# Optimization experiments

Hardware: AMD Instinct MI355X
Metric: run time of the kernel (lower is better)

The kernel has to match this reference:

```python
import jax, jax.numpy as jnp
import numpy as np

N = 100000   # nodes
E = 600000   # edges
D_IN, D_H, D_OUT = 128, 128, 128


def glorot(key, shape):
    lim = float(np.sqrt(6.0 / (shape[0] + shape[1])))
    return jax.random.uniform(key, shape, jnp.float32, -lim, lim)


def setup_inputs() -> dict:
    key = jax.random.key(0)
    k1, k2, k3, k4 = jax.random.split(key, 4)
    x = jax.random.normal(k1, (N, D_IN), jnp.float32)
    edge_index = jax.random.randint(k2, (2, E), 0, N, jnp.int64)
    W1 = glorot(k3, (D_IN, D_H))
    b1 = jnp.zeros((D_H,), jnp.float32)
    W2 = glorot(k4, (D_H, D_OUT))
    b2 = jnp.zeros((D_OUT,), jnp.float32)
    return {"x": x, "W1": W1, "b1": b1, "W2": W2, "b2": b2, "edge_index": edge_index}


def gcn_conv(x, W, b, src, dst, n):
    # GCNConv: D^{-1/2}(A+I)D^{-1/2} X W + b  (self loops already in src/dst)
    h = x @ W                                   # [N, d_out]
    ones = jnp.ones(src.shape[0], h.dtype)
    deg = jax.ops.segment_sum(ones, dst, num_segments=n)      # in-degree incl self loop
    dinv = jnp.where(deg > 0, jax.lax.rsqrt(deg), 0.0)        # deg^{-1/2}
    norm = dinv[src] * dinv[dst]                              # [E+N]
    msgs = h[src] * norm[:, None]                             # gather + scale
    out = jax.ops.segment_sum(msgs, dst, num_segments=n)      # scatter-add to targets
    return out + b


def reference(x, W1, b1, W2, b2, edge_index):
    loop = jnp.arange(N, dtype=edge_index.dtype)
    src = jnp.concatenate([edge_index[0], loop])
    dst = jnp.concatenate([edge_index[1], loop])
    h = gcn_conv(x, W1, b1, src, dst, N)
    h = jax.nn.relu(h)  # dropout is a no-op in eval mode
    return gcn_conv(h, W2, b2, src, dst, N)
```

## Files before the change

kernel.cpp:

```cpp
#include <hip/hip_runtime.h>

#define NFEAT 128

typedef __attribute__((ext_vector_type(8))) short bf16x8;
typedef __attribute__((ext_vector_type(4))) float f32x4;

__device__ inline ushort f2b(float v) {
  unsigned u = __builtin_bit_cast(unsigned, v);
  unsigned r = (u + 0x7FFFu + ((u >> 16) & 1u)) >> 16;
  return (ushort)r;
}


__global__ __launch_bounds__(256) void k_hist(const int* __restrict__ dst,
                                              int* __restrict__ cnt, int E) {
  int i = blockIdx.x * 256 + threadIdx.x;
  if (i < E) atomicAdd(&cnt[dst[i]], 1);
}

__global__ __launch_bounds__(256) void k_dinv(const int* __restrict__ cnt,
                                              float* __restrict__ dinv, int n) {
  int i = blockIdx.x * 256 + threadIdx.x;
  if (i < n) dinv[i] = rsqrtf((float)(cnt[i] + 1));
}

__global__ __launch_bounds__(256) void k_scan_blocks(const int* __restrict__ cnt,
                                                     int* __restrict__ rowptr,
                                                     int* __restrict__ bsum, int n) {
  __shared__ int s[256];
  int tid = threadIdx.x;
  int idx = blockIdx.x * 1024 + tid * 4;
  int v[4];
  int sum = 0;
#pragma unroll
  for (int j = 0; j < 4; j++) {
    v[j] = (idx + j < n) ? cnt[idx + j] : 0;
    sum += v[j];
  }
  s[tid] = sum;
  __syncthreads();
  for (int off = 1; off < 256; off <<= 1) {
    int t = (tid >= off) ? s[tid - off] : 0;
    __syncthreads();
    s[tid] += t;
    __syncthreads();
  }
  if (tid == 255) bsum[blockIdx.x] = s[255];
  int run = s[tid] - sum;
#pragma unroll
  for (int j = 0; j < 4; j++) {
    if (idx + j < n) rowptr[idx + j] = run;
    run += v[j];
  }
}

__global__ __launch_bounds__(128) void k_scan_sums(int* __restrict__ bsum, int nb) {
  __shared__ int s[128];
  int tid = threadIdx.x;
  int v = (tid < nb) ? bsum[tid] : 0;
  s[tid] = v;
  __syncthreads();
  for (int off = 1; off < 128; off <<= 1) {
    int t = (tid >= off) ? s[tid - off] : 0;
    __syncthreads();
    s[tid] += t;
    __syncthreads();
  }
  if (tid < nb) bsum[tid] = s[tid] - v;
}

__global__ __launch_bounds__(256) void k_scan_add(int* __restrict__ rowptr,
                                                  const int* __restrict__ bsum,
                                                  int n, int e_total) {
  int i = blockIdx.x * 256 + threadIdx.x;
  if (i < n) rowptr[i] += bsum[i >> 10];
  if (i == 0) rowptr[n] = e_total;
}

__global__ __launch_bounds__(256) void k_scatter(const int* __restrict__ src,
                                                 const int* __restrict__ dst,
                                                 const int* __restrict__ rowptr,
                                                 const float* __restrict__ dinv,
                                                 int* __restrict__ cursor,
                                                 int2* __restrict__ csr2, int E) {
  int i = blockIdx.x * 256 + threadIdx.x;
  if (i < E) {
    int d = dst[i];
    int s = src[i];
    int p = atomicAdd(&cursor[d], 1);
    int2 v;
    v.x = s;
    v.y = __float_as_int(dinv[s]);
    csr2[rowptr[d] + p] = v;
  }
}


__global__ __launch_bounds__(256) void k_cast_x(const float* __restrict__ x,
                                                ushort* __restrict__ xb, int total8) {
  int i = blockIdx.x * 256 + threadIdx.x;
  if (i >= total8) return;
  const float4* p = (const float4*)(x + (size_t)i * 8);
  float4 a = p[0], b = p[1];
  uint4 o;
  o.x = f2b(a.x) | ((unsigned)f2b(a.y) << 16);
  o.y = f2b(a.z) | ((unsigned)f2b(a.w) << 16);
  o.z = f2b(b.x) | ((unsigned)f2b(b.y) << 16);
  o.w = f2b(b.z) | ((unsigned)f2b(b.w) << 16);
  *(uint4*)(xb + (size_t)i * 8) = o;
}

__global__ __launch_bounds__(256) void k_cast_wt(const float* __restrict__ W,
                                                 ushort* __restrict__ WT) {
  int idx = blockIdx.x * 256 + threadIdx.x;
  int k = idx >> 7, nn = idx & 127;
  WT[nn * 128 + k] = f2b(W[idx]);
}


__global__ __launch_bounds__(256) void k_gemm_bf16(const ushort* __restrict__ A,
                                                   const ushort* __restrict__ WT,
                                                   ushort* __restrict__ out, int n) {
  __shared__ ushort sW[128][136];
  int tid = threadIdx.x;
  {
    int r = tid >> 1, hh = tid & 1;
    const uint4* srcp = (const uint4*)(WT + r * 128 + hh * 64);
    uint4* dstp = (uint4*)(&sW[r][hh * 64]);
#pragma unroll
    for (int j = 0; j < 8; j++) dstp[j] = srcp[j];
  }
  __syncthreads();

  int wave = tid >> 6;
  int lane = tid & 63;
  int l16 = lane & 15;
  int quad = lane >> 4;
  int rowBase = blockIdx.x * 128 + wave * 32;

  bf16x8 afrag[2][4];
#pragma unroll
  for (int rt = 0; rt < 2; rt++) {
    int row = rowBase + rt * 16 + l16;
    row = min(row, n - 1);
    const ushort* Ap = A + (size_t)row * NFEAT + quad * 8;
#pragma unroll
    for (int ks = 0; ks < 4; ks++) afrag[rt][ks] = *(const bf16x8*)(Ap + ks * 32);
  }

#pragma unroll
  for (int ct = 0; ct < 8; ct++) {
    bf16x8 bfrag[4];
#pragma unroll
    for (int ks = 0; ks < 4; ks++)
      bfrag[ks] = *(const bf16x8*)(&sW[ct * 16 + l16][ks * 32 + quad * 8]);
    f32x4 acc[2] = {{0.f, 0.f, 0.f, 0.f}, {0.f, 0.f, 0.f, 0.f}};
#pragma unroll
    for (int rt = 0; rt < 2; rt++)
#pragma unroll
      for (int ks = 0; ks < 4; ks++)
        acc[rt] = __builtin_amdgcn_mfma_f32_16x16x32_bf16(afrag[rt][ks], bfrag[ks],
                                                          acc[rt], 0, 0, 0);
#pragma unroll
    for (int rt = 0; rt < 2; rt++)
#pragma unroll
      for (int r = 0; r < 4; r++) {
        int row = rowBase + rt * 16 + quad * 4 + r;
        if (row < n) out[(size_t)row * NFEAT + ct * 16 + l16] = f2b(acc[rt][r]);
      }
  }
}


__global__ __launch_bounds__(256) void k_agg_bf16(const ushort* __restrict__ h,
                                                  const float* __restrict__ dinv,
                                                  const int* __restrict__ rowptr,
                                                  const int2* __restrict__ csr2,
                                                  const float* __restrict__ bias,
                                                  ushort* __restrict__ out_bf,
                                                  float* __restrict__ out_f32,
                                                  int n, int relu_bf) {
  int node = blockIdx.x * 8 + (threadIdx.x >> 5);
  if (node >= n) return;
  int lane = threadIdx.x & 31;
  int c = lane * 4;
  float di = dinv[node];

  uint2 hv = *(const uint2*)(h + (size_t)node * NFEAT + c);
  float a0 = di * __uint_as_float(hv.x << 16);
  float a1 = di * __uint_as_float(hv.x & 0xffff0000u);
  float a2 = di * __uint_as_float(hv.y << 16);
  float a3 = di * __uint_as_float(hv.y & 0xffff0000u);

  int e = rowptr[node], end = rowptr[node + 1];
  for (; e + 3 < end; e += 4) {
    int2 p0 = csr2[e], p1 = csr2[e + 1], p2 = csr2[e + 2], p3 = csr2[e + 3];
    uint2 h0 = *(const uint2*)(h + (size_t)p0.x * NFEAT + c);
    uint2 h1 = *(const uint2*)(h + (size_t)p1.x * NFEAT + c);
    uint2 h2 = *(const uint2*)(h + (size_t)p2.x * NFEAT + c);
    uint2 h3 = *(const uint2*)(h + (size_t)p3.x * NFEAT + c);
    float w0 = __int_as_float(p0.y), w1 = __int_as_float(p1.y);
    float w2 = __int_as_float(p2.y), w3 = __int_as_float(p3.y);
    a0 = fmaf(w0, __uint_as_float(h0.x << 16), a0);
    a1 = fmaf(w0, __uint_as_float(h0.x & 0xffff0000u), a1);
    a2 = fmaf(w0, __uint_as_float(h0.y << 16), a2);
    a3 = fmaf(w0, __uint_as_float(h0.y & 0xffff0000u), a3);
    a0 = fmaf(w1, __uint_as_float(h1.x << 16), a0);
    a1 = fmaf(w1, __uint_as_float(h1.x & 0xffff0000u), a1);
    a2 = fmaf(w1, __uint_as_float(h1.y << 16), a2);
    a3 = fmaf(w1, __uint_as_float(h1.y & 0xffff0000u), a3);
    a0 = fmaf(w2, __uint_as_float(h2.x << 16), a0);
    a1 = fmaf(w2, __uint_as_float(h2.x & 0xffff0000u), a1);
    a2 = fmaf(w2, __uint_as_float(h2.y << 16), a2);
    a3 = fmaf(w2, __uint_as_float(h2.y & 0xffff0000u), a3);
    a0 = fmaf(w3, __uint_as_float(h3.x << 16), a0);
    a1 = fmaf(w3, __uint_as_float(h3.x & 0xffff0000u), a1);
    a2 = fmaf(w3, __uint_as_float(h3.y << 16), a2);
    a3 = fmaf(w3, __uint_as_float(h3.y & 0xffff0000u), a3);
  }
  for (; e < end; ++e) {
    int2 p0 = csr2[e];
    uint2 h0 = *(const uint2*)(h + (size_t)p0.x * NFEAT + c);
    float w0 = __int_as_float(p0.y);
    a0 = fmaf(w0, __uint_as_float(h0.x << 16), a0);
    a1 = fmaf(w0, __uint_as_float(h0.x & 0xffff0000u), a1);
    a2 = fmaf(w0, __uint_as_float(h0.y << 16), a2);
    a3 = fmaf(w0, __uint_as_float(h0.y & 0xffff0000u), a3);
  }

  float4 b = *(const float4*)(bias + c);
  float o0 = fmaf(di, a0, b.x);
  float o1 = fmaf(di, a1, b.y);
  float o2 = fmaf(di, a2, b.z);
  float o3 = fmaf(di, a3, b.w);
  if (relu_bf) {
    o0 = fmaxf(o0, 0.f); o1 = fmaxf(o1, 0.f);
    o2 = fmaxf(o2, 0.f); o3 = fmaxf(o3, 0.f);
    uint2 pk;
    pk.x = f2b(o0) | ((unsigned)f2b(o1) << 16);
    pk.y = f2b(o2) | ((unsigned)f2b(o3) << 16);
    *(uint2*)(out_bf + (size_t)node * NFEAT + c) = pk;
  } else {
    float4 o = {o0, o1, o2, o3};
    *(float4*)(out_f32 + (size_t)node * NFEAT + c) = o;
  }
}


extern "C" void kernel_launch(void* const* d_in, const int* in_sizes, int n_in,
                              void* d_out, int out_size, void* d_ws, size_t ws_size,
                              hipStream_t stream) {
  const float* x = (const float*)d_in[0];
  const float* W1 = (const float*)d_in[1];
  const float* b1 = (const float*)d_in[2];
  const float* W2 = (const float*)d_in[3];
  const float* b2 = (const float*)d_in[4];
  const int* ei = (const int*)d_in[5];

  const int N = in_sizes[0] / NFEAT;
  const int E = in_sizes[5] / 2;
  const int* srcIdx = ei;
  const int* dstIdx = ei + E;

  char* p = (char*)d_ws;
  auto alloc = [&](size_t bytes) {
    char* r = p;
    p += (bytes + 255) & ~(size_t)255;
    return r;
  };
  int* cnt = (int*)alloc((size_t)N * 4);
  int* cursor = (int*)alloc((size_t)N * 4);
  float* dinv = (float*)alloc((size_t)N * 4);
  int* rowptr = (int*)alloc((size_t)(N + 1) * 4);
  int* bsum = (int*)alloc(512);
  int2* csr2 = (int2*)alloc((size_t)E * 8);
  ushort* WT1 = (ushort*)alloc(NFEAT * NFEAT * 2);
  ushort* WT2 = (ushort*)alloc(NFEAT * NFEAT * 2);
  ushort* t1 = (ushort*)alloc((size_t)N * NFEAT * 2);
  ushort* h2 = (ushort*)alloc((size_t)N * NFEAT * 2);
  ushort* xb = (ushort*)d_out;
  ushort* h1 = xb + (size_t)N * NFEAT;
  float* out = (float*)d_out;

  hipMemsetAsync(cnt, 0, (size_t)((char*)dinv - (char*)cnt), stream);

  int gE = (E + 255) / 256;
  int gN = (N + 255) / 256;
  int nb = (N + 1023) / 1024;

  k_hist<<<gE, 256, 0, stream>>>(dstIdx, cnt, E);
  k_dinv<<<gN, 256, 0, stream>>>(cnt, dinv, N);
  k_scan_blocks<<<nb, 256, 0, stream>>>(cnt, rowptr, bsum, N);
  k_scan_sums<<<1, 128, 0, stream>>>(bsum, nb);
  k_scan_add<<<gN, 256, 0, stream>>>(rowptr, bsum, N, E);
  k_scatter<<<gE, 256, 0, stream>>>(srcIdx, dstIdx, rowptr, dinv, cursor, csr2, E);

  k_cast_wt<<<64, 256, 0, stream>>>(W1, WT1);
  k_cast_wt<<<64, 256, 0, stream>>>(W2, WT2);
  int t8 = N * NFEAT / 8;
  k_cast_x<<<(t8 + 255) / 256, 256, 0, stream>>>(x, xb, t8);

  int gG = (N + 127) / 128;
  int gA = (N + 7) / 8;

  k_gemm_bf16<<<gG, 256, 0, stream>>>(xb, WT1, h1, N);
  k_agg_bf16<<<gA, 256, 0, stream>>>(h1, dinv, rowptr, csr2, b1, t1, nullptr, N, 1);
  k_gemm_bf16<<<gG, 256, 0, stream>>>(t1, WT2, h2, N);
  k_agg_bf16<<<gA, 256, 0, stream>>>(h2, dinv, rowptr, csr2, b2, nullptr, out, N, 0);
}
```

Measured before the change: 279.6 us.

## Fuse graph preprocessing kernels, pad CSR rows, and fold x cast into GEMM

Folds the fp32-to-bf16 cast of x into the first GEMM's fragment loads, removing a separate full pass over x. Merges dinv computation into the scan and the scan-sums/scan-add steps into one kernel that also seeds the cursor. Partitions the histogram and scatter atomics by destination range across blocks so atomics stay local. Pads each CSR row to a multiple of four with zeroed entries so the aggregation loop has no scalar tail. Costs extra CSR memory, a larger memset, and eight passes over the edge index arrays.

```diff
diff --git a/kernel.cpp b/kernel.cpp
--- a/kernel.cpp
+++ b/kernel.cpp
@@ -7,26 +7,30 @@
 
 __device__ inline ushort f2b(float v) {
   unsigned u = __builtin_bit_cast(unsigned, v);
-  unsigned r = (u + 0x7FFFu + ((u >> 16) & 1u)) >> 16;
-  return (ushort)r;
+  return (ushort)((u + 0x7FFFu + ((u >> 16) & 1u)) >> 16);
 }
 
 
 __global__ __launch_bounds__(256) void k_hist(const int* __restrict__ dst,
-                                              int* __restrict__ cnt, int E) {
-  int i = blockIdx.x * 256 + threadIdx.x;
-  if (i < E) atomicAdd(&cnt[dst[i]], 1);
-}
-
-__global__ __launch_bounds__(256) void k_dinv(const int* __restrict__ cnt,
-                                              float* __restrict__ dinv, int n) {
-  int i = blockIdx.x * 256 + threadIdx.x;
-  if (i < n) dinv[i] = rsqrtf((float)(cnt[i] + 1));
+                                              int* __restrict__ cnt, int E, int N) {
+  int range = blockIdx.x & 7, chunk = blockIdx.x >> 3;
+  int lo = (int)(((long long)range * N) >> 3);
+  int hi = (int)(((long long)(range + 1) * N) >> 3);
+  int base = chunk * 1024;
+#pragma unroll
+  for (int j = 0; j < 4; j++) {
+    int i = base + j * 256 + threadIdx.x;
+    if (i < E) {
+      int d = dst[i];
+      if ((unsigned)(d - lo) < (unsigned)(hi - lo)) atomicAdd(&cnt[d], 1);
+    }
+  }
 }
 
 __global__ __launch_bounds__(256) void k_scan_blocks(const int* __restrict__ cnt,
                                                      int* __restrict__ rowptr,
-                                                     int* __restrict__ bsum, int n) {
+                                                     int* __restrict__ bsum,
+                                                     float* __restrict__ dinv, int n) {
   __shared__ int s[256];
   int tid = threadIdx.x;
   int idx = blockIdx.x * 1024 + tid * 4;
@@ -34,7 +38,12 @@
   int sum = 0;
 #pragma unroll
   for (int j = 0; j < 4; j++) {
-    v[j] = (idx + j < n) ? cnt[idx + j] : 0;
+    int c = 0;
+    if (idx + j < n) {
+      c = cnt[idx + j];
+      dinv[idx + j] = rsqrtf((float)(c + 1));
+    }
+    v[j] = (idx + j < n) ? ((c + 3) & ~3) : 0;
     sum += v[j];
   }
   s[tid] = sum;
@@ -54,73 +63,79 @@
   }
 }
 
-__global__ __launch_bounds__(128) void k_scan_sums(int* __restrict__ bsum, int nb) {
-  __shared__ int s[128];
+__global__ __launch_bounds__(256) void k_scan_addcur(int* __restrict__ rowptr,
+                                                     const int* __restrict__ bsum,
+                                                     int* __restrict__ cursor,
+                                                     int n, int nb) {
+  __shared__ int s[256];
   int tid = threadIdx.x;
   int v = (tid < nb) ? bsum[tid] : 0;
   s[tid] = v;
   __syncthreads();
-  for (int off = 1; off < 128; off <<= 1) {
+  for (int off = 1; off < 256; off <<= 1) {
     int t = (tid >= off) ? s[tid - off] : 0;
     __syncthreads();
     s[tid] += t;
     __syncthreads();
   }
-  if (tid < nb) bsum[tid] = s[tid] - v;
-}
-
-__global__ __launch_bounds__(256) void k_scan_add(int* __restrict__ rowptr,
-                                                  const int* __restrict__ bsum,
-                                                  int n, int e_total) {
-  int i = blockIdx.x * 256 + threadIdx.x;
-  if (i < n) rowptr[i] += bsum[i >> 10];
-  if (i == 0) rowptr[n] = e_total;
+  int total = s[255];
+  __syncthreads();
+  int ex = s[tid] - v;
+  __syncthreads();
+  s[tid] = ex;
+  __syncthreads();
+  int i = blockIdx.x * 256 + tid;
+  if (i < n) {
+    int rp = rowptr[i] + s[i >> 10];
+    rowptr[i] = rp;
+    cursor[i] = rp;
+  }
+  if (i == 0) rowptr[n] = total;
 }
 
 __global__ __launch_bounds__(256) void k_scatter(const int* __restrict__ src,
                                                  const int* __restrict__ dst,
-                                                 const int* __restrict__ rowptr,
                                                  const float* __restrict__ dinv,
                                                  int* __restrict__ cursor,
-                                                 int2* __restrict__ csr2, int E) {
-  int i = blockIdx.x * 256 + threadIdx.x;
-  if (i < E) {
-    int d = dst[i];
-    int s = src[i];
-    int p = atomicAdd(&cursor[d], 1);
-    int2 v;
-    v.x = s;
-    v.y = __float_as_int(dinv[s]);
-    csr2[rowptr[d] + p] = v;
-  }
-}
-
-
-__global__ __launch_bounds__(256) void k_cast_x(const float* __restrict__ x,
-                                                ushort* __restrict__ xb, int total8) {
-  int i = blockIdx.x * 256 + threadIdx.x;
-  if (i >= total8) return;
-  const float4* p = (const float4*)(x + (size_t)i * 8);
-  float4 a = p[0], b = p[1];
-  uint4 o;
-  o.x = f2b(a.x) | ((unsigned)f2b(a.y) << 16);
-  o.y = f2b(a.z) | ((unsigned)f2b(a.w) << 16);
-  o.z = f2b(b.x) | ((unsigned)f2b(b.y) << 16);
-  o.w = f2b(b.z) | ((unsigned)f2b(b.w) << 16);
-  *(uint4*)(xb + (size_t)i * 8) = o;
-}
-
-__global__ __launch_bounds__(256) void k_cast_wt(const float* __restrict__ W,
-                                                 ushort* __restrict__ WT) {
-  int idx = blockIdx.x * 256 + threadIdx.x;
+                                                 int2* __restrict__ csr2, int E, int N) {
+  int range = blockIdx.x & 7, chunk = blockIdx.x >> 3;
+  int lo = (int)(((long long)range * N) >> 3);
+  int hi = (int)(((long long)(range + 1) * N) >> 3);
+  int base = chunk * 1024;
+#pragma unroll
+  for (int j = 0; j < 4; j++) {
+    int i = base + j * 256 + threadIdx.x;
+    if (i < E) {
+      int d = dst[i];
+      if ((unsigned)(d - lo) < (unsigned)(hi - lo)) {
+        int s = src[i];
+        int p = atomicAdd(&cursor[d], 1);
+        int2 v;
+        v.x = s;
+        v.y = __float_as_int(dinv[s]);
+        csr2[p] = v;
+      }
+    }
+  }
+}
+
+__global__ __launch_bounds__(256) void k_cast_w(const float* __restrict__ W1,
+                                                const float* __restrict__ W2,
+                                                ushort* __restrict__ WT1,
+                                                ushort* __restrict__ WT2) {
+  int b = blockIdx.x;
+  const float* W = (b < 64) ? W1 : W2;
+  ushort* WT = (b < 64) ? WT1 : WT2;
+  int idx = (b & 63) * 256 + threadIdx.x;
   int k = idx >> 7, nn = idx & 127;
   WT[nn * 128 + k] = f2b(W[idx]);
 }
 
 
-__global__ __launch_bounds__(256) void k_gemm_bf16(const ushort* __restrict__ A,
-                                                   const ushort* __restrict__ WT,
-                                                   ushort* __restrict__ out, int n) {
+template <bool AFP32>
+__global__ __launch_bounds__(256) void k_gemm(const void* __restrict__ Av,
+                                              const ushort* __restrict__ WT,
+                                              ushort* __restrict__ out, int n) {
   __shared__ ushort sW[128][136];
   int tid = threadIdx.x;
   {
@@ -143,9 +158,21 @@
   for (int rt = 0; rt < 2; rt++) {
     int row = rowBase + rt * 16 + l16;
     row = min(row, n - 1);
-    const ushort* Ap = A + (size_t)row * NFEAT + quad * 8;
-#pragma unroll
-    for (int ks = 0; ks < 4; ks++) afrag[rt][ks] = *(const bf16x8*)(Ap + ks * 32);
+    if (AFP32) {
+      const float* Ap = (const float*)Av + (size_t)row * NFEAT + quad * 8;
+#pragma unroll
+      for (int ks = 0; ks < 4; ks++) {
+        float4 f0 = *(const float4*)(Ap + ks * 32);
+        float4 f1 = *(const float4*)(Ap + ks * 32 + 4);
+        ushort t[8] = {f2b(f0.x), f2b(f0.y), f2b(f0.z), f2b(f0.w),
+                       f2b(f1.x), f2b(f1.y), f2b(f1.z), f2b(f1.w)};
+        afrag[rt][ks] = *(const bf16x8*)t;
+      }
+    } else {
+      const ushort* Ap = (const ushort*)Av + (size_t)row * NFEAT + quad * 8;
+#pragma unroll
+      for (int ks = 0; ks < 4; ks++) afrag[rt][ks] = *(const bf16x8*)(Ap + ks * 32);
+    }
   }
 
 #pragma unroll
@@ -172,18 +199,17 @@
 }
 
 
-__global__ __launch_bounds__(256) void k_agg_bf16(const ushort* __restrict__ h,
-                                                  const float* __restrict__ dinv,
-                                                  const int* __restrict__ rowptr,
-                                                  const int2* __restrict__ csr2,
-                                                  const float* __restrict__ bias,
-                                                  ushort* __restrict__ out_bf,
-                                                  float* __restrict__ out_f32,
-                                                  int n, int relu_bf) {
+__global__ __launch_bounds__(256) void k_agg(const ushort* __restrict__ h,
+                                             const float* __restrict__ dinv,
+                                             const int* __restrict__ rowptr,
+                                             const int2* __restrict__ csr2,
+                                             const float* __restrict__ bias,
+                                             ushort* __restrict__ out_bf,
+                                             float* __restrict__ out_f32,
+                                             int n, int relu_bf) {
   int node = blockIdx.x * 8 + (threadIdx.x >> 5);
   if (node >= n) return;
-  int lane = threadIdx.x & 31;
-  int c = lane * 4;
+  int c = (threadIdx.x & 31) * 4;
   float di = dinv[node];
 
   uint2 hv = *(const uint2*)(h + (size_t)node * NFEAT + c);
@@ -193,7 +219,7 @@
   float a3 = di * __uint_as_float(hv.y & 0xffff0000u);
 
   int e = rowptr[node], end = rowptr[node + 1];
-  for (; e + 3 < end; e += 4) {
+  for (; e < end; e += 4) {
     int2 p0 = csr2[e], p1 = csr2[e + 1], p2 = csr2[e + 2], p3 = csr2[e + 3];
     uint2 h0 = *(const uint2*)(h + (size_t)p0.x * NFEAT + c);
     uint2 h1 = *(const uint2*)(h + (size_t)p1.x * NFEAT + c);
@@ -218,15 +244,6 @@
     a2 = fmaf(w3, __uint_as_float(h3.y << 16), a2);
     a3 = fmaf(w3, __uint_as_float(h3.y & 0xffff0000u), a3);
   }
-  for (; e < end; ++e) {
-    int2 p0 = csr2[e];
-    uint2 h0 = *(const uint2*)(h + (size_t)p0.x * NFEAT + c);
-    float w0 = __int_as_float(p0.y);
-    a0 = fmaf(w0, __uint_as_float(h0.x << 16), a0);
-    a1 = fmaf(w0, __uint_as_float(h0.x & 0xffff0000u), a1);
-    a2 = fmaf(w0, __uint_as_float(h0.y << 16), a2);
-    a3 = fmaf(w0, __uint_as_float(h0.y & 0xffff0000u), a3);
-  }
 
   float4 b = *(const float4*)(bias + c);
   float o0 = fmaf(di, a0, b.x);
@@ -269,42 +286,35 @@
     return r;
   };
   int* cnt = (int*)alloc((size_t)N * 4);
+  int2* csr2 = (int2*)alloc((size_t)(E + 3 * N + 8) * 8);
+  char* memset_end = p;
   int* cursor = (int*)alloc((size_t)N * 4);
   float* dinv = (float*)alloc((size_t)N * 4);
   int* rowptr = (int*)alloc((size_t)(N + 1) * 4);
-  int* bsum = (int*)alloc(512);
-  int2* csr2 = (int2*)alloc((size_t)E * 8);
+  int* bsum = (int*)alloc(1024);
   ushort* WT1 = (ushort*)alloc(NFEAT * NFEAT * 2);
   ushort* WT2 = (ushort*)alloc(NFEAT * NFEAT * 2);
   ushort* t1 = (ushort*)alloc((size_t)N * NFEAT * 2);
   ushort* h2 = (ushort*)alloc((size_t)N * NFEAT * 2);
-  ushort* xb = (ushort*)d_out;
-  ushort* h1 = xb + (size_t)N * NFEAT;
+  ushort* h1 = (ushort*)d_out;
   float* out = (float*)d_out;
 
-  hipMemsetAsync(cnt, 0, (size_t)((char*)dinv - (char*)cnt), stream);
-
-  int gE = (E + 255) / 256;
-  int gN = (N + 255) / 256;
+  hipMemsetAsync(cnt, 0, (size_t)(memset_end - (char*)cnt), stream);
+
   int nb = (N + 1023) / 1024;
-
-  k_hist<<<gE, 256, 0, stream>>>(dstIdx, cnt, E);
-  k_dinv<<<gN, 256, 0, stream>>>(cnt, dinv, N);
-  k_scan_blocks<<<nb, 256, 0, stream>>>(cnt, rowptr, bsum, N);
-  k_scan_sums<<<1, 128, 0, stream>>>(bsum, nb);
-  k_scan_add<<<gN, 256, 0, stream>>>(rowptr, bsum, N, E);
-  k_scatter<<<gE, 256, 0, stream>>>(srcIdx, dstIdx, rowptr, dinv, cursor, csr2, E);
-
-  k_cast_wt<<<64, 256, 0, stream>>>(W1, WT1);
-  k_cast_wt<<<64, 256, 0, stream>>>(W2, WT2);
-  int t8 = N * NFEAT / 8;
-  k_cast_x<<<(t8 + 255) / 256, 256, 0, stream>>>(x, xb, t8);
+  int gEx = ((E + 1023) / 1024) * 8;
+
+  k_hist<<<gEx, 256, 0, stream>>>(dstIdx, cnt, E, N);
+  k_scan_blocks<<<nb, 256, 0, stream>>>(cnt, rowptr, bsum, dinv, N);
+  k_scan_addcur<<<(N + 255) / 256, 256, 0, stream>>>(rowptr, bsum, cursor, N, nb);
+  k_scatter<<<gEx, 256, 0, stream>>>(srcIdx, dstIdx, dinv, cursor, csr2, E, N);
+  k_cast_w<<<128, 256, 0, stream>>>(W1, W2, WT1, WT2);
 
   int gG = (N + 127) / 128;
   int gA = (N + 7) / 8;
 
-  k_gemm_bf16<<<gG, 256, 0, stream>>>(xb, WT1, h1, N);
-  k_agg_bf16<<<gA, 256, 0, stream>>>(h1, dinv, rowptr, csr2, b1, t1, nullptr, N, 1);
-  k_gemm_bf16<<<gG, 256, 0, stream>>>(t1, WT2, h2, N);
-  k_agg_bf16<<<gA, 256, 0, stream>>>(h2, dinv, rowptr, csr2, b2, nullptr, out, N, 0);
-}
+  k_gemm<true><<<gG, 256, 0, stream>>>(x, WT1, h1, N);
+  k_agg<<<gA, 256, 0, stream>>>(h1, dinv, rowptr, csr2, b1, t1, nullptr, N, 1);
+  k_gemm<false><<<gG, 256, 0, stream>>>(t1, WT2, h2, N);
+  k_agg<<<gA, 256, 0, stream>>>(h2, dinv, rowptr, csr2, b2, nullptr, out, N, 0);
+}
```

Result: faster. 262.6 us (-6.0%).
